# Optimization experiments

Measured on AMD Instinct MI355X. Metric: run time of the kernel, lower is better.

## Reference

```python
import jax, jax.numpy as jnp
import numpy as np

D_MODEL, D_STATE, D_INNER, DT_RANK, D_CONV, K = 768, 16, 1536, 48, 3, 2
B_SZ, L_SEQ = 2, 2048

def setup_inputs() -> dict:
    key = jax.random.key(0)
    ks = jax.random.split(key, 10)
    s = lambda k, shp, sc=0.02: jax.random.normal(k, shp, dtype=jnp.float32) * sc
    return {
        "x": jax.random.normal(ks[0], (B_SZ, L_SEQ, D_MODEL), dtype=jnp.float32),
        "in_proj_w": s(ks[1], (2 * D_INNER, D_MODEL)),
        "conv_w": s(ks[2], (D_INNER, 1, D_CONV), 0.3),
        "conv_b": s(ks[3], (D_INNER,), 0.1),
        "x_proj_w": s(ks[4], (K, DT_RANK + 2 * D_STATE, D_INNER)),
        "dt_proj_w": s(ks[5], (K, D_INNER, DT_RANK), 0.1),
        "dt_proj_b": s(ks[6], (K, D_INNER), 0.1),
        "A_logs": s(ks[7], (K * D_INNER, D_STATE), 0.5),
        "Ds": jnp.ones((K * D_INNER,), dtype=jnp.float32),
        "out_proj_w": s(ks[8], (D_MODEL, D_INNER)),
    }

def _selective_scan(u, delta, A, Bp, Cp, Dk):
    # u, delta: [B, L, D]; A: [D, N]; Bp, Cp: [B, L, N]; Dk: [D]
    def step(h, inp):
        d_t, u_t, b_t, c_t = inp  # [B,D], [B,D], [B,N], [B,N]
        dA = jnp.exp(d_t[..., None] * A)  # [B,D,N]
        h = h * dA + (d_t * u_t)[..., None] * b_t[:, None, :]
        y_t = jnp.einsum('bdn,bn->bd', h, c_t)
        return h, y_t
    h0 = jnp.zeros((u.shape[0], u.shape[2], A.shape[1]), dtype=u.dtype)
    xs = (jnp.swapaxes(delta, 0, 1), jnp.swapaxes(u, 0, 1),
          jnp.swapaxes(Bp, 0, 1), jnp.swapaxes(Cp, 0, 1))
    _, ys = jax.lax.scan(step, h0, xs)  # ys: [L, B, D]
    return jnp.swapaxes(ys, 0, 1) + u * Dk  # [B, L, D]

def _direction(u_k, xw_k, dtw_k, dtb_k, Alog_k, D_k):
    x_dbl = jnp.einsum('bld,rd->blr', u_k, xw_k)
    dt_in, Bp, Cp = jnp.split(x_dbl, [DT_RANK, DT_RANK + D_STATE], axis=-1)
    delta = jax.nn.softplus(jnp.einsum('blr,dr->bld', dt_in, dtw_k) + dtb_k)
    A = -jnp.exp(Alog_k)
    return _selective_scan(u_k, delta, A, Bp, Cp, D_k)

def reference(x, in_proj_w, conv_w, conv_b, x_proj_w, dt_proj_w, dt_proj_b, A_logs, Ds, out_proj_w):
    xz = x @ in_proj_w.T                       # [B, L, 2*Din]
    x_conv, z = jnp.split(xz, 2, axis=-1)
    xc = jnp.swapaxes(x_conv, 1, 2)            # [B, Din, L]
    pad = (D_CONV - 1) // 2
    xc = jax.lax.conv_general_dilated(
        xc, conv_w, window_strides=(1,), padding=[(pad, pad)],
        feature_group_count=D_INNER, dimension_numbers=('NCH', 'OIH', 'NCH'))
    xc = xc + conv_b[None, :, None]
    u = jnp.swapaxes(jax.nn.silu(xc), 1, 2)    # [B, L, Din]

    u_dirs = jnp.stack([u, jnp.flip(u, axis=1)])          # [K, B, L, Din]
    A_logs_k = A_logs.reshape(K, D_INNER, D_STATE)
    Ds_k = Ds.reshape(K, D_INNER)
    y_dirs = jax.vmap(_direction)(u_dirs, x_proj_w, dt_proj_w, dt_proj_b, A_logs_k, Ds_k)
    y_scanned = y_dirs[0] + jnp.flip(y_dirs[1], axis=1)
    y_gated = y_scanned * z
    return y_gated @ out_proj_w.T
```

## Files before the change

kernel.cpp:

```cpp
#include <hip/hip_runtime.h>
#include <math.h>

#define D_MODEL 768
#define D_STATE 16
#define D_INNER 1536
#define DT_RANK 48
#define B_SZ    2
#define L_SEQ   2048
#define CH      64
#define NCH     (L_SEQ / CH)
#define NDG     24
#define MTOT    (B_SZ * L_SEQ)
#define LOG2E   1.4426950408889634f
#define LN2     0.6931471805599453f

typedef __bf16 bf16x8 __attribute__((ext_vector_type(8)));
typedef float f32x4 __attribute__((ext_vector_type(4)));
typedef ushort ushort8_t __attribute__((ext_vector_type(8)));

__device__ __forceinline__ float ex2(float x) {
  return __builtin_amdgcn_exp2f(x);
}

__device__ __forceinline__ ushort f2bf(float f) {
  unsigned int u = __float_as_uint(f);
  unsigned int r = (u + 0x7fff + ((u >> 16) & 1)) >> 16;
  return (ushort)r;
}
__device__ __forceinline__ float bf2f(ushort u) {
  return __uint_as_float(((unsigned int)u) << 16);
}

__device__ __forceinline__ void gload_lds16(const ushort* g, ushort* l) {
  __builtin_amdgcn_global_load_lds(
      (__attribute__((address_space(1))) void*)(void*)(g),
      (__attribute__((address_space(3))) void*)(void*)(l), 16, 0, 0);
}

__device__ __forceinline__ float softplus_fast(float x) {
  return (x > 20.f) ? x : LN2 * __log2f(1.f + ex2(x * LOG2E));
}

template <int BM, int BN, int ACT, int OBF, int DTOUT>
__device__ __forceinline__ void gemm_body(
    const ushort* __restrict__ A, int lda, const ushort* __restrict__ B,
    int ldb, const float* __restrict__ bias, void* __restrict__ Cp, int ldc,
    int Nreal, int K, int bxi, int byi, ushort* __restrict__ dtin) {
  __shared__ ushort As[2][BM][32];
  __shared__ ushort Bs[2][BN][32];
  constexpr int WM = BM / 2, WN = BN / 2;
  constexpr int FM = WM / 16, FN = WN / 16;
  const int tid = threadIdx.x;
  const int lane = tid & 63;
  const int w = tid >> 6;
  const int wr = w >> 1, wc = w & 1;
  const int bm = byi * BM, bn = bxi * BN;
  const int lrow = lane >> 2;
  const int lchunk = lane & 3;
  const int fr = lane & 15;
  const int k8 = (lane >> 4) * 8;

  f32x4 acc[FM][FN] = {};

  auto stage = [&](int buf, int k0) {
#pragma unroll
    for (int g = 0; g < BM / 64; ++g) {
      const int rb = w * (BM / 4) + g * 16;
      gload_lds16(A + (size_t)(bm + rb + lrow) * lda + k0 + lchunk * 8,
                  &As[buf][rb][0]);
    }
#pragma unroll
    for (int g = 0; g < BN / 64; ++g) {
      const int rb = w * (BN / 4) + g * 16;
      gload_lds16(B + (size_t)(bn + rb + lrow) * ldb + k0 + lchunk * 8,
                  &Bs[buf][rb][0]);
    }
  };

  stage(0, 0);
  __syncthreads();
  int cur = 0;
  for (int k0 = 0; k0 < K; k0 += 32) {
    if (k0 + 32 < K) stage(cur ^ 1, k0 + 32);
    bf16x8 af[FM], bfr[FN];
#pragma unroll
    for (int m = 0; m < FM; ++m)
      af[m] =
          *reinterpret_cast<const bf16x8*>(&As[cur][wr * WM + m * 16 + fr][k8]);
#pragma unroll
    for (int n = 0; n < FN; ++n)
      bfr[n] =
          *reinterpret_cast<const bf16x8*>(&Bs[cur][wc * WN + n * 16 + fr][k8]);
#pragma unroll
    for (int m = 0; m < FM; ++m)
#pragma unroll
      for (int n = 0; n < FN; ++n)
        acc[m][n] = __builtin_amdgcn_mfma_f32_16x16x32_bf16(af[m], bfr[n],
                                                            acc[m][n], 0, 0, 0);
    __syncthreads();
    cur ^= 1;
  }

  const int row4 = (lane >> 4) * 4;
#pragma unroll
  for (int m = 0; m < FM; ++m) {
#pragma unroll
    for (int n = 0; n < FN; ++n) {
      const int gn = bn + wc * WN + n * 16 + fr;
      const int gm0 = bm + wr * WM + m * 16 + row4;
#pragma unroll
      for (int j = 0; j < 4; ++j) {
        const float v = acc[m][n][j];
        const int gm = gm0 + j;
        if (DTOUT) {
          if (gn < 64)
            dtin[(size_t)gm * 64 + gn] = (gn < 48) ? f2bf(v) : (ushort)0;
          else if (gn >= 80 && gn < 144)
            dtin[(size_t)MTOT * 64 + (size_t)gm * 64 + (gn - 80)] =
                (gn < 128) ? f2bf(v) : (ushort)0;
        }
        if (gn < Nreal) {
          float vv = v + (bias ? bias[gn] : 0.f);
          if (ACT == 1) vv = softplus_fast(vv);
          if (OBF)
            ((ushort*)Cp)[(size_t)gm * ldc + gn] = f2bf(vv);
          else
            ((float*)Cp)[(size_t)gm * ldc + gn] = vv;
        }
      }
    }
  }
}

template <int BM, int BN, int ACT, int OBF, int DTOUT>
__global__ __launch_bounds__(256) void gemm_k(
    const ushort* __restrict__ A, int lda, const ushort* __restrict__ B,
    int ldb, const float* __restrict__ bias, void* __restrict__ Cp, int ldc,
    int Nreal, int K, ushort* __restrict__ dtin) {
  gemm_body<BM, BN, ACT, OBF, DTOUT>(A, lda, B, ldb, bias, Cp, ldc, Nreal, K,
                                     blockIdx.x, blockIdx.y, dtin);
}

__global__ __launch_bounds__(256) void gemm_dt_k(
    const ushort* __restrict__ dtin, const ushort* __restrict__ w_dt,
    const float* __restrict__ dtb, ushort* __restrict__ delta) {
  const int k = blockIdx.z;
  gemm_body<64, 128, 1, 1, 0>(
      dtin + (size_t)k * MTOT * 64, 64, w_dt + (size_t)k * D_INNER * 64, 64,
      dtb + k * D_INNER, delta + (size_t)k * MTOT * D_INNER, D_INNER, D_INNER,
      64, blockIdx.x, blockIdx.y, nullptr);
}

__global__ __launch_bounds__(256) void cvt_all_kernel(
    const float* __restrict__ x, const float* __restrict__ w_in,
    const float* __restrict__ w_out, const float* __restrict__ w_xp,
    const float* __restrict__ w_dt, ushort* __restrict__ x_bf,
    ushort* __restrict__ w_in_bf, ushort* __restrict__ w_out_bf,
    ushort* __restrict__ w_xp_bf, ushort* __restrict__ w_dt_bf) {
  const long N0 = 3145728, N1 = 2359296, N2 = 1179648, N3 = 393216, N4 = 196608;
  long i = ((long)blockIdx.x * 256 + threadIdx.x) * 4;
  if (i < N0) {
    const float4 v = *(const float4*)(x + i);
    ushort4 o = {f2bf(v.x), f2bf(v.y), f2bf(v.z), f2bf(v.w)};
    *(ushort4*)(x_bf + i) = o;
    return;
  }
  i -= N0;
  if (i < N1) {
    const float4 v = *(const float4*)(w_in + i);
    ushort4 o = {f2bf(v.x), f2bf(v.y), f2bf(v.z), f2bf(v.w)};
    *(ushort4*)(w_in_bf + i) = o;
    return;
  }
  i -= N1;
  if (i < N2) {
    const float4 v = *(const float4*)(w_out + i);
    ushort4 o = {f2bf(v.x), f2bf(v.y), f2bf(v.z), f2bf(v.w)};
    *(ushort4*)(w_out_bf + i) = o;
    return;
  }
  i -= N2;
  if (i < N3) {
    const long row = i / 1536;
    ushort4 o = {0, 0, 0, 0};
    if (row < 160) {
      const float4 v = *(const float4*)(w_xp + i);
      o.x = f2bf(v.x); o.y = f2bf(v.y); o.z = f2bf(v.z); o.w = f2bf(v.w);
    }
    *(ushort4*)(w_xp_bf + i) = o;
    return;
  }
  i -= N3;
  if (i < N4) {
    const int col = (int)(i & 63);
    const long row = i >> 6;
    ushort4 o = {0, 0, 0, 0};
    if (col < 48) {
      const float4 v = *(const float4*)(w_dt + row * 48 + col);
      o.x = f2bf(v.x); o.y = f2bf(v.y); o.z = f2bf(v.z); o.w = f2bf(v.w);
    }
    *(ushort4*)(w_dt_bf + i) = o;
  }
}

__global__ __launch_bounds__(256) void conv_silu_kernel(
    const ushort* __restrict__ xz, const float* __restrict__ cw,
    const float* __restrict__ cb, ushort* __restrict__ u_bf) {
  const int nd8 = D_INNER / 8;
  int idx = blockIdx.x * 256 + threadIdx.x;
  if (idx >= B_SZ * L_SEQ * nd8) return;
  const int d = (idx % nd8) * 8;
  const int l = (idx / nd8) % L_SEQ;
  const int b = idx / (nd8 * L_SEQ);
  float a[8];
#pragma unroll
  for (int j8 = 0; j8 < 8; ++j8) a[j8] = cb[d + j8];
#pragma unroll
  for (int j = 0; j < 3; ++j) {
    const int ll = l + j - 1;
    if (ll < 0 || ll >= L_SEQ) continue;
    const ushort8_t xv =
        *(const ushort8_t*)(xz + ((size_t)b * L_SEQ + ll) * 3072 + d);
#pragma unroll
    for (int j8 = 0; j8 < 8; ++j8)
      a[j8] += bf2f(xv[j8]) * cw[(d + j8) * 3 + j];
  }
  ushort8_t o;
#pragma unroll
  for (int j8 = 0; j8 < 8; ++j8) {
    const float s = a[j8] / (1.f + __expf(-a[j8]));
    o[j8] = f2bf(s);
  }
  *(ushort8_t*)(u_bf + ((size_t)b * L_SEQ + l) * D_INNER + d) = o;
}

__global__ __launch_bounds__(256) void scan_local_kernel(
    const ushort* __restrict__ u_bf, const float* __restrict__ xdbl,
    const ushort* __restrict__ delta_bf, const float* __restrict__ A_logs,
    const float* __restrict__ Ds, ushort* __restrict__ y,
    float* __restrict__ hfin, float* __restrict__ Tsum) {
  __shared__ float sd[32][64], su[32][64], sB[32][16], sC[32][16];
  const int tid = threadIdx.x;
  const int lane = tid & 63;
  const int w = tid >> 6;
  const int c = lane & 15;
  const int nq = lane >> 4;
  const int bid = blockIdx.x;
  const int ch = bid & (NCH - 1);
  const int rest = bid >> 5;
  const int dgB = rest % NDG;
  const int kb = rest / NDG;
  const int b = kb & 1;
  const int k = kb >> 1;
  const int d0 = dgB * 64;
  const int dl = w * 16 + c;
  const int d = d0 + dl;
  const int row = k * D_INNER + d;

  const float4 alv = *(const float4*)(A_logs + (size_t)row * D_STATE + nq * 4);
  const float An0 = -__expf(alv.x) * LOG2E, An1 = -__expf(alv.y) * LOG2E;
  const float An2 = -__expf(alv.z) * LOG2E, An3 = -__expf(alv.w) * LOG2E;
  const float Dk = Ds[row];

  const ushort* uptr = u_bf + ((size_t)b * L_SEQ) * D_INNER;
  const ushort* dptr = delta_bf + ((size_t)(k * B_SZ + b) * L_SEQ) * D_INNER;
  const float* xptr = xdbl + ((size_t)b * L_SEQ) * 160 + k * 80;
  ushort* yptr = y + ((size_t)(k * B_SZ + b) * L_SEQ) * D_INNER;

  float h0 = 0.f, h1 = 0.f, h2 = 0.f, h3 = 0.f, S = 0.f;

  for (int sub = 0; sub < CH / 32; ++sub) {
    const int t0 = ch * CH + sub * 32;
    const int lbase = k ? (L_SEQ - 32 - t0) : t0;
    {
      const int r = tid >> 3, seg = tid & 7;
      const int ridx = k ? (31 - r) : r;
      const size_t off = (size_t)(lbase + r) * D_INNER + d0 + seg * 8;
      const ushort8_t dv = *(const ushort8_t*)(dptr + off);
      const ushort8_t uv = *(const ushort8_t*)(uptr + off);
      *(float4*)&sd[ridx][seg * 8] =
          make_float4(bf2f(dv[0]), bf2f(dv[1]), bf2f(dv[2]), bf2f(dv[3]));
      *(float4*)&sd[ridx][seg * 8 + 4] =
          make_float4(bf2f(dv[4]), bf2f(dv[5]), bf2f(dv[6]), bf2f(dv[7]));
      *(float4*)&su[ridx][seg * 8] =
          make_float4(bf2f(uv[0]), bf2f(uv[1]), bf2f(uv[2]), bf2f(uv[3]));
      *(float4*)&su[ridx][seg * 8 + 4] =
          make_float4(bf2f(uv[4]), bf2f(uv[5]), bf2f(uv[6]), bf2f(uv[7]));
    }
    {
      const int t2 = tid & 127;
      const int r = t2 >> 2;
      const int ridx = k ? (31 - r) : r;
      const int c4 = (t2 & 3) * 4;
      const size_t rowL = (size_t)(lbase + r);
      if (tid < 128)
        *(float4*)&sB[ridx][c4] =
            *(const float4*)(xptr + rowL * 160 + DT_RANK + c4);
      else
        *(float4*)&sC[ridx][c4] =
            *(const float4*)(xptr + rowL * 160 + DT_RANK + D_STATE + c4);
    }
    __syncthreads();
    for (int s = 0; s < 32; ++s) {
      const float dlt = sd[s][dl];
      const float uu = su[s][dl];
      S += dlt;
      const float4 Bv = *(const float4*)&sB[s][nq * 4];
      const float4 Cv = *(const float4*)&sC[s][nq * 4];
      const float du = dlt * uu;
      h0 = h0 * ex2(dlt * An0) + du * Bv.x;
      h1 = h1 * ex2(dlt * An1) + du * Bv.y;
      h2 = h2 * ex2(dlt * An2) + du * Bv.z;
      h3 = h3 * ex2(dlt * An3) + du * Bv.w;
      float yt = h0 * Cv.x + h1 * Cv.y + h2 * Cv.z + h3 * Cv.w;
      yt += __shfl_xor(yt, 16);
      yt += __shfl_xor(yt, 32);
      if (nq == 0) {
        const int t = t0 + s;
        const int l = k ? (L_SEQ - 1 - t) : t;
        yptr[(size_t)l * D_INNER + d] = f2bf(yt + uu * Dk);
      }
    }
    __syncthreads();
  }

  const size_t cidxB = ((size_t)(k * B_SZ + b) * NCH + ch) * NDG + dgB;
  *(float4*)(hfin + cidxB * 1024 + dl * 16 + nq * 4) =
      make_float4(h0, h1, h2, h3);
  if (nq == 0) Tsum[cidxB * 64 + dl] = S;
}

__global__ __launch_bounds__(256) void scan_stitch_kernel(
    const float* __restrict__ hfin, const float* __restrict__ Tsum,
    const float* __restrict__ A_logs, float* __restrict__ hin) {
  const int tid = threadIdx.x;
  const int dl = tid >> 2;
  const int nq = tid & 3;
  const int bid = blockIdx.x;
  const int dgB = bid % NDG;
  const int b = (bid / NDG) & 1;
  const int k = bid / (NDG * 2);
  const int row = k * D_INNER + dgB * 64 + dl;
  const float4 alv = *(const float4*)(A_logs + (size_t)row * D_STATE + nq * 4);
  const float An0 = -__expf(alv.x) * LOG2E, An1 = -__expf(alv.y) * LOG2E;
  const float An2 = -__expf(alv.z) * LOG2E, An3 = -__expf(alv.w) * LOG2E;
  float c0 = 0.f, c1 = 0.f, c2 = 0.f, c3 = 0.f;
  for (int ch = 0; ch < NCH; ++ch) {
    const size_t cidxB = ((size_t)(k * B_SZ + b) * NCH + ch) * NDG + dgB;
    const size_t off = cidxB * 1024 + dl * 16 + nq * 4;
    *(float4*)(hin + off) = make_float4(c0, c1, c2, c3);
    const float T = Tsum[cidxB * 64 + dl];
    const float4 hf = *(const float4*)(hfin + off);
    c0 = c0 * ex2(An0 * T) + hf.x;
    c1 = c1 * ex2(An1 * T) + hf.y;
    c2 = c2 * ex2(An2 * T) + hf.z;
    c3 = c3 * ex2(An3 * T) + hf.w;
  }
}

__global__ __launch_bounds__(256) void fixup_gate_kernel(
    const float* __restrict__ xdbl, const ushort* __restrict__ delta_bf,
    const float* __restrict__ A_logs, const float* __restrict__ hin,
    const ushort* __restrict__ y, const ushort* __restrict__ xz_bf,
    ushort* __restrict__ yg) {
  __shared__ float sd0[64][64], sd1[64][64];
  __shared__ float sC0[64][16], sC1[64][16];
  __shared__ float sQF[64][4], sQB[64][4];
  const int tid = threadIdx.x;
  const int tq = tid >> 6;
  const int dl = tid & 63;
  const int bid = blockIdx.x;
  const int ch = bid & (NCH - 1);
  const int rest = bid >> 5;
  const int dgB = rest % NDG;
  const int b = rest / NDG;
  const int d0 = dgB * 64;
  const int d = d0 + dl;
  const int lbase = ch * CH;
  const int chb = NCH - 1 - ch;

  float AnF[16], AnB[16], hF[16], hB[16];
#pragma unroll
  for (int q = 0; q < 4; ++q) {
    const float4 af = *(const float4*)(A_logs + (size_t)d * D_STATE + q * 4);
    AnF[q * 4 + 0] = -__expf(af.x) * LOG2E;
    AnF[q * 4 + 1] = -__expf(af.y) * LOG2E;
    AnF[q * 4 + 2] = -__expf(af.z) * LOG2E;
    AnF[q * 4 + 3] = -__expf(af.w) * LOG2E;
    const float4 ab =
        *(const float4*)(A_logs + (size_t)(D_INNER + d) * D_STATE + q * 4);
    AnB[q * 4 + 0] = -__expf(ab.x) * LOG2E;
    AnB[q * 4 + 1] = -__expf(ab.y) * LOG2E;
    AnB[q * 4 + 2] = -__expf(ab.z) * LOG2E;
    AnB[q * 4 + 3] = -__expf(ab.w) * LOG2E;
  }
  const size_t cF = ((size_t)(0 * B_SZ + b) * NCH + ch) * NDG + dgB;
  const size_t cB = ((size_t)(1 * B_SZ + b) * NCH + chb) * NDG + dgB;
#pragma unroll
  for (int q = 0; q < 4; ++q) {
    const float4 hv = *(const float4*)(hin + cF * 1024 + dl * 16 + q * 4);
    hF[q * 4 + 0] = hv.x; hF[q * 4 + 1] = hv.y;
    hF[q * 4 + 2] = hv.z; hF[q * 4 + 3] = hv.w;
    const float4 hw = *(const float4*)(hin + cB * 1024 + dl * 16 + q * 4);
    hB[q * 4 + 0] = hw.x; hB[q * 4 + 1] = hw.y;
    hB[q * 4 + 2] = hw.z; hB[q * 4 + 3] = hw.w;
  }

  const ushort* d0p =
      delta_bf + ((size_t)(0 * B_SZ + b) * L_SEQ + lbase) * D_INNER + d0;
  const ushort* d1p =
      delta_bf + ((size_t)(1 * B_SZ + b) * L_SEQ + lbase) * D_INNER + d0;
#pragma unroll
  for (int i = 0; i < 2; ++i) {
    const int unit = tid + i * 256;
    const int r = unit >> 3, seg = unit & 7;
    const ushort8_t v0 =
        *(const ushort8_t*)(d0p + (size_t)r * D_INNER + seg * 8);
    const ushort8_t v1 =
        *(const ushort8_t*)(d1p + (size_t)r * D_INNER + seg * 8);
    *(float4*)&sd0[r][seg * 8] =
        make_float4(bf2f(v0[0]), bf2f(v0[1]), bf2f(v0[2]), bf2f(v0[3]));
    *(float4*)&sd0[r][seg * 8 + 4] =
        make_float4(bf2f(v0[4]), bf2f(v0[5]), bf2f(v0[6]), bf2f(v0[7]));
    *(float4*)&sd1[r][seg * 8] =
        make_float4(bf2f(v1[0]), bf2f(v1[1]), bf2f(v1[2]), bf2f(v1[3]));
    *(float4*)&sd1[r][seg * 8 + 4] =
        make_float4(bf2f(v1[4]), bf2f(v1[5]), bf2f(v1[6]), bf2f(v1[7]));
  }
  {
    const int r = tid >> 2;
    const int c4 = (tid & 3) * 4;
    const float* xrow = xdbl + ((size_t)b * L_SEQ + lbase + r) * 160;
    *(float4*)&sC0[r][c4] = *(const float4*)(xrow + DT_RANK + D_STATE + c4);
    *(float4*)&sC1[r][c4] =
        *(const float4*)(xrow + 80 + DT_RANK + D_STATE + c4);
  }
  __syncthreads();
  float qf = 0.f, qb = 0.f;
#pragma unroll
  for (int i = 0; i < 16; ++i) {
    qf += sd0[tq * 16 + i][dl];
    qb += sd1[tq * 16 + i][dl];
  }
  sQF[dl][tq] = qf;
  sQB[dl][tq] = qb;
  __syncthreads();
  float SF = 0.f, SB = 0.f;
#pragma unroll
  for (int j = 0; j < 4; ++j) {
    if (j < tq) SF += sQF[dl][j];
    if (j > tq) SB += sQB[dl][j];
  }

  const ushort* y0p = y + ((size_t)(0 * B_SZ + b) * L_SEQ) * D_INNER;
  const ushort* y1p = y + ((size_t)(1 * B_SZ + b) * L_SEQ) * D_INNER;
  float yacc[16];
#pragma unroll
  for (int i = 0; i < 16; ++i) {
    const int t = tq * 16 + i;
    SF += sd0[t][dl];
    float wf = 0.f;
#pragma unroll
    for (int n = 0; n < 16; ++n)
      wf += sC0[t][n] * (ex2(AnF[n] * SF) * hF[n]);
    yacc[i] = bf2f(y0p[(size_t)(lbase + t) * D_INNER + d]) + wf;
  }
#pragma unroll
  for (int i = 15; i >= 0; --i) {
    const int t = tq * 16 + i;
    SB += sd1[t][dl];
    float wb = 0.f;
#pragma unroll
    for (int n = 0; n < 16; ++n)
      wb += sC1[t][n] * (ex2(AnB[n] * SB) * hB[n]);
    yacc[i] += bf2f(y1p[(size_t)(lbase + t) * D_INNER + d]) + wb;
  }
#pragma unroll
  for (int i = 0; i < 16; ++i) {
    const int l = lbase + tq * 16 + i;
    const float z = bf2f(xz_bf[((size_t)b * L_SEQ + l) * 3072 + 1536 + d]);
    yg[((size_t)b * L_SEQ + l) * D_INNER + d] = f2bf(yacc[i] * z);
  }
}

extern "C" void kernel_launch(void* const* d_in, const int* in_sizes, int n_in,
                              void* d_out, int out_size, void* d_ws,
                              size_t ws_size, hipStream_t stream) {
  const float* x          = (const float*)d_in[0];
  const float* in_proj_w  = (const float*)d_in[1];
  const float* conv_w     = (const float*)d_in[2];
  const float* conv_b     = (const float*)d_in[3];
  const float* x_proj_w   = (const float*)d_in[4];
  const float* dt_proj_w  = (const float*)d_in[5];
  const float* dt_proj_b  = (const float*)d_in[6];
  const float* A_logs     = (const float*)d_in[7];
  const float* Ds         = (const float*)d_in[8];
  const float* out_proj_w = (const float*)d_in[9];
  float* out = (float*)d_out;

  const int M = MTOT;
  const size_t NST = (size_t)2 * B_SZ * NCH * NDG;

  float* ws    = (float*)d_ws;
  float* xdbl  = ws;
  float* hfin  = xdbl + (size_t)M * 160;
  float* hin   = hfin + NST * 1024;
  float* Tsum  = hin + NST * 1024;
  ushort* x_bf     = (ushort*)(Tsum + NST * 64);
  ushort* w_in_bf  = x_bf + (size_t)M * 768;
  ushort* w_out_bf = w_in_bf + (size_t)3072 * 768;
  ushort* w_xp_bf  = w_out_bf + (size_t)768 * 1536;
  ushort* w_dt_bf  = w_xp_bf + (size_t)256 * 1536;
  ushort* xz_bf    = w_dt_bf + (size_t)2 * 1536 * 64;
  ushort* u_bf     = xz_bf + (size_t)M * 3072;
  ushort* delta_bf = u_bf + (size_t)M * 1536;
  ushort* dtin     = delta_bf + (size_t)2 * M * 1536;
  ushort* y_bf     = dtin + (size_t)2 * M * 64;
  ushort* yg_bf    = y_bf + (size_t)2 * M * 1536;

  dim3 blk(256);

  {
    const long TOT = 3145728L + 2359296 + 1179648 + 393216 + 196608;
    cvt_all_kernel<<<dim3((TOT / 4 + 255) / 256), blk, 0, stream>>>(
        x, in_proj_w, out_proj_w, x_proj_w, dt_proj_w, x_bf, w_in_bf, w_out_bf,
        w_xp_bf, w_dt_bf);
  }

  gemm_k<128, 128, 0, 1, 0><<<dim3(3072 / 128, M / 128), blk, 0, stream>>>(
      x_bf, 768, w_in_bf, 768, nullptr, xz_bf, 3072, 3072, 768, nullptr);

  conv_silu_kernel<<<dim3(M * (D_INNER / 8) / 256), blk, 0, stream>>>(
      xz_bf, conv_w, conv_b, u_bf);

  gemm_k<64, 64, 0, 0, 1><<<dim3(256 / 64, M / 64), blk, 0, stream>>>(
      u_bf, 1536, w_xp_bf, 1536, nullptr, xdbl, 160, 160, 1536, dtin);

  gemm_dt_k<<<dim3(1536 / 128, M / 64, 2), blk, 0, stream>>>(
      dtin, w_dt_bf, dt_proj_b, delta_bf);

  scan_local_kernel<<<dim3(2 * B_SZ * NDG * NCH), blk, 0, stream>>>(
      u_bf, xdbl, delta_bf, A_logs, Ds, y_bf, hfin, Tsum);
  scan_stitch_kernel<<<dim3(2 * B_SZ * NDG), blk, 0, stream>>>(hfin, Tsum,
                                                               A_logs, hin);
  fixup_gate_kernel<<<dim3(B_SZ * NDG * NCH), blk, 0, stream>>>(
      xdbl, delta_bf, A_logs, hin, y_bf, xz_bf, yg_bf);

  gemm_k<128, 128, 0, 0, 0><<<dim3(768 / 128, M / 128), blk, 0, stream>>>(
      yg_bf, 1536, w_out_bf, 1536, nullptr, out, 768, 768, 1536, nullptr);
}
```

Baseline: 250.4 us.

## Register-block conv over sequence, prefetch scan chunks, trim x_proj grid

The conv+SiLU kernel now has each thread compute 8 consecutive positions with a sliding window of loaded rows, so each xz row is read about once rather than three times and the weights are loaded once per thread. The local scan kernel prefetches the next 32-step sub-chunk of delta, u, B and C into registers while the current one is computed, overlapping global loads with the recurrence. The x_proj GEMM grid drops from 4 to 3 column tiles, skipping a tile past the 160 used columns. The conv change cuts thread count by 8x, which lowers parallelism, and the prefetch adds register pressure.

```diff
diff --git a/kernel.cpp b/kernel.cpp
--- a/kernel.cpp
+++ b/kernel.cpp
@@ -207,31 +207,41 @@
     const ushort* __restrict__ xz, const float* __restrict__ cw,
     const float* __restrict__ cb, ushort* __restrict__ u_bf) {
   const int nd8 = D_INNER / 8;
-  int idx = blockIdx.x * 256 + threadIdx.x;
-  if (idx >= B_SZ * L_SEQ * nd8) return;
-  const int d = (idx % nd8) * 8;
-  const int l = (idx / nd8) % L_SEQ;
-  const int b = idx / (nd8 * L_SEQ);
-  float a[8];
-#pragma unroll
-  for (int j8 = 0; j8 < 8; ++j8) a[j8] = cb[d + j8];
-#pragma unroll
-  for (int j = 0; j < 3; ++j) {
-    const int ll = l + j - 1;
-    if (ll < 0 || ll >= L_SEQ) continue;
-    const ushort8_t xv =
-        *(const ushort8_t*)(xz + ((size_t)b * L_SEQ + ll) * 3072 + d);
-#pragma unroll
-    for (int j8 = 0; j8 < 8; ++j8)
-      a[j8] += bf2f(xv[j8]) * cw[(d + j8) * 3 + j];
-  }
-  ushort8_t o;
-#pragma unroll
-  for (int j8 = 0; j8 < 8; ++j8) {
-    const float s = a[j8] / (1.f + __expf(-a[j8]));
-    o[j8] = f2bf(s);
-  }
-  *(ushort8_t*)(u_bf + ((size_t)b * L_SEQ + l) * D_INNER + d) = o;
+  const int idx = blockIdx.x * 256 + threadIdx.x;
+  const int d8 = idx % nd8;
+  const int lg = (idx / nd8) % (L_SEQ / 8);
+  const int b = idx / (nd8 * (L_SEQ / 8));
+  const int d = d8 * 8;
+  const int l0 = lg * 8;
+
+  float w0[8], w1[8], w2[8], bs[8];
+#pragma unroll
+  for (int j = 0; j < 8; ++j) {
+    w0[j] = cw[(d + j) * 3 + 0];
+    w1[j] = cw[(d + j) * 3 + 1];
+    w2[j] = cw[(d + j) * 3 + 2];
+    bs[j] = cb[d + j];
+  }
+  const ushort* base = xz + ((size_t)b * L_SEQ) * 3072 + d;
+  const ushort8_t zv = {0, 0, 0, 0, 0, 0, 0, 0};
+  ushort8_t prev = (l0 > 0) ? *(const ushort8_t*)(base + (size_t)(l0 - 1) * 3072) : zv;
+  ushort8_t curv = *(const ushort8_t*)(base + (size_t)l0 * 3072);
+#pragma unroll
+  for (int i = 0; i < 8; ++i) {
+    const int l = l0 + i;
+    const ushort8_t nxt =
+        (l + 1 < L_SEQ) ? *(const ushort8_t*)(base + (size_t)(l + 1) * 3072) : zv;
+    ushort8_t o;
+#pragma unroll
+    for (int j = 0; j < 8; ++j) {
+      const float a = bs[j] + bf2f(prev[j]) * w0[j] + bf2f(curv[j]) * w1[j] +
+                      bf2f(nxt[j]) * w2[j];
+      o[j] = f2bf(a / (1.f + __expf(-a)));
+    }
+    *(ushort8_t*)(u_bf + ((size_t)b * L_SEQ + l) * D_INNER + d) = o;
+    prev = curv;
+    curv = nxt;
+  }
 }
 
 __global__ __launch_bounds__(256) void scan_local_kernel(
@@ -267,40 +277,47 @@
   const float* xptr = xdbl + ((size_t)b * L_SEQ) * 160 + k * 80;
   ushort* yptr = y + ((size_t)(k * B_SZ + b) * L_SEQ) * D_INNER;
 
-  float h0 = 0.f, h1 = 0.f, h2 = 0.f, h3 = 0.f, S = 0.f;
-
-  for (int sub = 0; sub < CH / 32; ++sub) {
+  const int r_st = tid >> 3, seg = tid & 7;
+  const int ridx_st = k ? (31 - r_st) : r_st;
+  const int t2 = tid & 127;
+  const int rBC = t2 >> 2;
+  const int ridx_bc = k ? (31 - rBC) : rBC;
+  const int c4 = (t2 & 3) * 4;
+  const bool isB = tid < 128;
+
+  ushort8_t dv, uv;
+  float4 bc;
+  auto gload = [&](int sub) {
     const int t0 = ch * CH + sub * 32;
     const int lbase = k ? (L_SEQ - 32 - t0) : t0;
-    {
-      const int r = tid >> 3, seg = tid & 7;
-      const int ridx = k ? (31 - r) : r;
-      const size_t off = (size_t)(lbase + r) * D_INNER + d0 + seg * 8;
-      const ushort8_t dv = *(const ushort8_t*)(dptr + off);
-      const ushort8_t uv = *(const ushort8_t*)(uptr + off);
-      *(float4*)&sd[ridx][seg * 8] =
-          make_float4(bf2f(dv[0]), bf2f(dv[1]), bf2f(dv[2]), bf2f(dv[3]));
-      *(float4*)&sd[ridx][seg * 8 + 4] =
-          make_float4(bf2f(dv[4]), bf2f(dv[5]), bf2f(dv[6]), bf2f(dv[7]));
-      *(float4*)&su[ridx][seg * 8] =
-          make_float4(bf2f(uv[0]), bf2f(uv[1]), bf2f(uv[2]), bf2f(uv[3]));
-      *(float4*)&su[ridx][seg * 8 + 4] =
-          make_float4(bf2f(uv[4]), bf2f(uv[5]), bf2f(uv[6]), bf2f(uv[7]));
-    }
-    {
-      const int t2 = tid & 127;
-      const int r = t2 >> 2;
-      const int ridx = k ? (31 - r) : r;
-      const int c4 = (t2 & 3) * 4;
-      const size_t rowL = (size_t)(lbase + r);
-      if (tid < 128)
-        *(float4*)&sB[ridx][c4] =
-            *(const float4*)(xptr + rowL * 160 + DT_RANK + c4);
-      else
-        *(float4*)&sC[ridx][c4] =
-            *(const float4*)(xptr + rowL * 160 + DT_RANK + D_STATE + c4);
-    }
+    const size_t off = (size_t)(lbase + r_st) * D_INNER + d0 + seg * 8;
+    dv = *(const ushort8_t*)(dptr + off);
+    uv = *(const ushort8_t*)(uptr + off);
+    const size_t rowL = (size_t)(lbase + rBC);
+    bc = isB ? *(const float4*)(xptr + rowL * 160 + DT_RANK + c4)
+             : *(const float4*)(xptr + rowL * 160 + DT_RANK + D_STATE + c4);
+  };
+
+  gload(0);
+
+  float h0 = 0.f, h1 = 0.f, h2 = 0.f, h3 = 0.f, S = 0.f;
+
+  for (int sub = 0; sub < CH / 32; ++sub) {
+    *(float4*)&sd[ridx_st][seg * 8] =
+        make_float4(bf2f(dv[0]), bf2f(dv[1]), bf2f(dv[2]), bf2f(dv[3]));
+    *(float4*)&sd[ridx_st][seg * 8 + 4] =
+        make_float4(bf2f(dv[4]), bf2f(dv[5]), bf2f(dv[6]), bf2f(dv[7]));
+    *(float4*)&su[ridx_st][seg * 8] =
+        make_float4(bf2f(uv[0]), bf2f(uv[1]), bf2f(uv[2]), bf2f(uv[3]));
+    *(float4*)&su[ridx_st][seg * 8 + 4] =
+        make_float4(bf2f(uv[4]), bf2f(uv[5]), bf2f(uv[6]), bf2f(uv[7]));
+    if (isB)
+      *(float4*)&sB[ridx_bc][c4] = bc;
+    else
+      *(float4*)&sC[ridx_bc][c4] = bc;
     __syncthreads();
+    if (sub + 1 < CH / 32) gload(sub + 1);
+    const int t0 = ch * CH + sub * 32;
     for (int s = 0; s < 32; ++s) {
       const float dlt = sd[s][dl];
       const float uu = su[s][dl];
@@ -530,10 +547,10 @@
   gemm_k<128, 128, 0, 1, 0><<<dim3(3072 / 128, M / 128), blk, 0, stream>>>(
       x_bf, 768, w_in_bf, 768, nullptr, xz_bf, 3072, 3072, 768, nullptr);
 
-  conv_silu_kernel<<<dim3(M * (D_INNER / 8) / 256), blk, 0, stream>>>(
-      xz_bf, conv_w, conv_b, u_bf);
-
-  gemm_k<64, 64, 0, 0, 1><<<dim3(256 / 64, M / 64), blk, 0, stream>>>(
+  conv_silu_kernel<<<dim3(B_SZ * (L_SEQ / 8) * (D_INNER / 8) / 256), blk, 0,
+                     stream>>>(xz_bf, conv_w, conv_b, u_bf);
+
+  gemm_k<64, 64, 0, 0, 1><<<dim3(3, M / 64), blk, 0, stream>>>(
       u_bf, 1536, w_xp_bf, 1536, nullptr, xdbl, 160, 160, 1536, dtin);
 
   gemm_dt_k<<<dim3(1536 / 128, M / 64, 2), blk, 0, stream>>>(
```

Result: faster. 228.7 us (-8.7%).
